# Optimization experiments

Measured on AMD Instinct MI355X. Metric: run time of the kernel, lower is better.

Reference implementation:

```python
import jax, jax.numpy as jnp
import numpy as np

TAU = 2.0   # LIF membrane time constant
VTH = 1.0   # spike threshold
EPS = 1e-5
T = 2       # spiking timesteps
H = 8       # attention heads
L = 4       # transformer depth
SCALE = 0.125
GW = 0.8    # graph branch weight


def _spike(v):
    # heaviside forward, sigmoid surrogate backward (spikingjelly-style)
    sg = jax.nn.sigmoid(4.0 * (v - VTH))
    return sg + jax.lax.stop_gradient((v >= VTH).astype(v.dtype) - sg)


def lif(x):
    # multi-step LIF over leading time axis, hard reset, detach_reset=True
    def step(v, xt):
        v = v + (xt - v) / TAU
        s = _spike(v)
        v = v * (1.0 - jax.lax.stop_gradient(s))
        return v, s
    _, s = jax.lax.scan(step, jnp.zeros_like(x[0]), x)
    return s


def bn(x, g, b):
    # batch-norm (training stats) over all dims but the channel dim
    ax = tuple(range(x.ndim - 1))
    m = x.mean(ax, keepdims=True)
    v = x.var(ax, keepdims=True)
    return (x - m) * jax.lax.rsqrt(v + EPS) * g + b


def ln(x, g, b):
    m = x.mean(-1, keepdims=True)
    v = x.var(-1, keepdims=True)
    return (x - m) * jax.lax.rsqrt(v + EPS) * g + b


def gcn_agg(x, row, col, n):
    # symmetric-normalized sparse aggregation: out[col] += x[row] / sqrt(d[row]d[col])
    deg = jax.ops.segment_sum(jnp.ones_like(col, dtype=x.dtype), col, num_segments=n)
    dinv = jnp.where(deg > 0, jax.lax.rsqrt(deg), 0.0)
    val = dinv[col] * dinv[row]
    return jax.ops.segment_sum(val[:, None] * x[row], col, num_segments=n)


def _forward(fl, edge_index):
    (x, fc0_w, fc0_b, ln_g, ln_b, wq, wk, wv, wo,
     bnq_g, bnq_b, bnk_g, bnk_b, bnv_g, bnv_b, bno_g, bno_b,
     w1, bn1_g, bn1_b, w2, bn2_g, bn2_b, head_w, head_b,
     gfc_w, gfc_b, gbn0_g, gbn0_b, gconv_w, gconv_b, gbn_g, gbn_b,
     fc_w, fc_b) = fl
    N = x.shape[0]
    row, col = edge_index[0], edge_index[1]
    # ---- spiking transformer branch: x -> [T,N,D] ----
    h = jnp.broadcast_to(x, (T,) + x.shape) @ fc0_w + fc0_b
    h = jax.nn.relu(ln(h, ln_g, ln_b))
    D = h.shape[-1]
    for l in range(L):
        s = lif(h)
        q = lif(bn(s @ wq[l], bnq_g[l], bnq_b[l])).reshape(T, N, H, D // H)
        k = lif(bn(s @ wk[l], bnk_g[l], bnk_b[l])).reshape(T, N, H, D // H)
        v = lif(bn(s @ wv[l], bnv_g[l], bnv_b[l])).reshape(T, N, H, D // H)
        # linear (token-sum) spiking self-attention: kv = K^T V per head/timestep
        kv = jnp.einsum('tnhd,tnhe->thde', k, v)
        o = (jnp.einsum('tnhd,thde->tnhe', q, kv) * SCALE).reshape(T, N, D)
        o = bn(lif(o) @ wo[l], bno_g[l], bno_b[l])
        h = h + o
        m = bn(lif(h) @ w1[l], bn1_g[l], bn1_b[l])
        m = bn(lif(m) @ w2[l], bn2_g[l], bn2_b[l])
        h = h + m
    x1 = (lif(h) @ head_w + head_b).mean(0)   # [N, C], mean over T (TET=False)
    # ---- sparse GNN diffusion branch ----
    g0 = jax.nn.relu(bn(x @ gfc_w + gfc_b, gbn0_g, gbn0_b))
    g = g0
    for i in range(2):
        g = gcn_agg(g, row, col, N) @ gconv_w[i] + gconv_b[i]
        g = jax.nn.relu(bn(g, gbn_g[i], gbn_b[i]))
        g = g + g0  # residual to first layer
    out = GW * g + (1.0 - GW) * x1
    return out @ fc_w + fc_b


def setup_inputs() -> dict:
    key = jax.random.key(0)
    ks = iter(jax.random.split(key, 64))
    N, F, D, C = 16384, 512, 512, 40
    DH = 2 * D
    r = lambda *s: jax.random.normal(next(ks), s, dtype=jnp.float32)
    inp = {
        'x': r(N, F),
        'fc0_w': r(F, D) * 0.02, 'fc0_b': jnp.zeros((D,), jnp.float32),
        'ln_g': jnp.ones((D,), jnp.float32), 'ln_b': jnp.zeros((D,), jnp.float32),
        'wq': r(L, D, D) * 0.02, 'wk': r(L, D, D) * 0.02,
        'wv': r(L, D, D) * 0.02, 'wo': r(L, D, D) * 0.02,
        'bnq_g': 1.0 + 0.1 * r(L, D), 'bnq_b': 0.02 * r(L, D),
        'bnk_g': 1.0 + 0.1 * r(L, D), 'bnk_b': 0.02 * r(L, D),
        'bnv_g': 1.0 + 0.1 * r(L, D), 'bnv_b': 0.02 * r(L, D),
        'bno_g': 1.0 + 0.1 * r(L, D), 'bno_b': 0.02 * r(L, D),
        'w1': r(L, D, DH) * 0.02, 'bn1_g': 1.0 + 0.1 * r(L, DH), 'bn1_b': 0.02 * r(L, DH),
        'w2': r(L, DH, D) * 0.02, 'bn2_g': 1.0 + 0.1 * r(L, D), 'bn2_b': 0.02 * r(L, D),
        'head_w': r(D, C) * 0.02, 'head_b': jnp.zeros((C,), jnp.float32),
        'gfc_w': r(F, C) * 0.02, 'gfc_b': jnp.zeros((C,), jnp.float32),
        'gbn0_g': jnp.ones((C,), jnp.float32), 'gbn0_b': jnp.zeros((C,), jnp.float32),
        'gconv_w': r(2, C, C) * 0.1, 'gconv_b': jnp.zeros((2, C), jnp.float32),
        'gbn_g': 1.0 + 0.1 * r(2, C), 'gbn_b': 0.02 * r(2, C),
        'fc_w': r(C, C) * 0.1, 'fc_b': jnp.zeros((C,), jnp.float32),
        'edge_index': jax.random.randint(next(ks), (2, 262144), 0, N, dtype=jnp.int32),
    }
    return inp


def reference(x, fc0_w, fc0_b, ln_g, ln_b, wq, wk, wv, wo, bnq_g, bnq_b, bnk_g, bnk_b, bnv_g, bnv_b, bno_g, bno_b, w1, bn1_g, bn1_b, w2, bn2_g, bn2_b, head_w, head_b, gfc_w, gfc_b, gbn0_g, gbn0_b, gconv_w, gconv_b, gbn_g, gbn_b, fc_w, fc_b, edge_index):
    fl = (x, fc0_w, fc0_b, ln_g, ln_b, wq, wk, wv, wo, bnq_g, bnq_b, bnk_g, bnk_b, bnv_g, bnv_b, bno_g, bno_b, w1, bn1_g, bn1_b, w2, bn2_g, bn2_b, head_w, head_b, gfc_w, gfc_b, gbn0_g, gbn0_b, gconv_w, gconv_b, gbn_g, gbn_b, fc_w, fc_b)
    return _forward(fl, edge_index)
```

## Files before the change

### kernel.cpp

```cpp
#include <hip/hip_runtime.h>
#include <cstddef>
#include <cstdint>

constexpr int N_NODES = 16384;
constexpr int D_MODEL = 512;
constexpr int C_OUT   = 40;
constexpr int CW      = 256;
constexpr int ND      = N_NODES * D_MODEL;
constexpr int M2      = 2 * N_NODES;

typedef int i32x4 __attribute__((ext_vector_type(4)));

#define S0 0.001953125
#define S1 1.52587890625e-05
#define S2 1.1920928955078125e-07
#define S3 9.31322574615478515625e-10
#define S4 7.2759576141834259033203125e-12

#define WD_Q 0
#define WD_K 1310720
#define WD_V 2621440
#define WD_O 3932160
#define WD_1 5242880
#define WD_2 7864320
#define WD_TOTAL 10485760

__global__ __launch_bounds__(256)
void w_digits_layer(const float* __restrict__ wq, const float* __restrict__ wk,
                    const float* __restrict__ wv, const float* __restrict__ wo,
                    const float* __restrict__ w1, const float* __restrict__ w2,
                    uint8_t* __restrict__ Wd) {
    int idx = blockIdx.x * 256 + threadIdx.x;
    const float* W;
    uint8_t* outb;
    int N, rem;
    if (idx < 65536) {
        int mm = idx >> 14;
        rem = idx & 16383;
        const float* ptrs[4] = {wq, wk, wv, wo};
        W = ptrs[mm]; outb = Wd + (size_t)mm * 1310720; N = 512;
    } else if (idx < 98304) {
        rem = idx - 65536; W = w1; outb = Wd + WD_1; N = 1024;
    } else {
        rem = idx - 98304; W = w2; outb = Wd + WD_2; N = 512;
    }
    int kg = rem / N, n = rem - kg * N;
    const float* Wp = W + (size_t)kg * 16 * N + n;
    uint8_t* out = outb + (size_t)(kg * N + n) * 80;
    const double scl[5] = {512.0, 65536.0, 8388608.0, 1073741824.0, 137438953472.0};
    const double inv[5] = {S0, S1, S2, S3, S4};
    union { uint8_t b[5][16]; i32x4 v[5]; } db;
#pragma unroll
    for (int kk = 0; kk < 16; ++kk) {
        double r = (double)Wp[(size_t)kk * N];
#pragma unroll
        for (int j = 0; j < 5; ++j) {
            int d = (int)rint(r * scl[j]);
            d = d > 127 ? 127 : (d < -127 ? -127 : d);
            r -= (double)d * inv[j];
            db.b[j][kk] = (uint8_t)(int8_t)d;
        }
    }
#pragma unroll
    for (int j = 0; j < 5; ++j)
        *reinterpret_cast<i32x4*>(out + j * 16) = db.v[j];
}

__global__ __launch_bounds__(256)
void gemm_i8_bits(const uint64_t* __restrict__ bits, int kWords,
                  const uint8_t* __restrict__ Wd, int Nmat, int colOff,
                  double* __restrict__ C, int ldc, int K,
                  double* __restrict__ sum, double* __restrict__ sumsq) {
    __shared__ __attribute__((aligned(16))) uint8_t Bs[20480];
    const int lane = threadIdx.x & 63;
    const int wv   = threadIdx.x >> 6;
    const int m    = lane & 15;
    const int q    = lane >> 4;
    const int rowT = blockIdx.y * 128 + wv * 32;
    const int colB = blockIdx.x * 64;

    i32x4 acc[2][4][5];
#pragma unroll
    for (int rt = 0; rt < 2; ++rt)
#pragma unroll
        for (int t = 0; t < 4; ++t)
#pragma unroll
            for (int j = 0; j < 5; ++j) acc[rt][t][j] = (i32x4){0, 0, 0, 0};

    const uint64_t* brow0 = bits + (size_t)(rowT + m) * kWords;
    const uint64_t* brow1 = brow0 + (size_t)16 * kWords;
    const size_t cb = (size_t)(colOff + colB);

    for (int kb = 0; kb < K; kb += 64) {
        i32x4 tmp[5];
        const size_t kt0 = (size_t)(kb >> 4);
#pragma unroll
        for (int c5 = 0; c5 < 5; ++c5) {
            int c  = threadIdx.x + c5 * 256;
            int kt = c / 320;
            int of = c - kt * 320;
            tmp[c5] = *reinterpret_cast<const i32x4*>(
                Wd + ((kt0 + (size_t)kt) * Nmat + cb) * 80 + (size_t)of * 16);
        }
        uint64_t wb0 = brow0[kb >> 6];
        uint64_t wb1 = brow1[kb >> 6];
        uint32_t hw0 = (uint32_t)(wb0 >> (q * 16)) & 0xFFFFu;
        uint32_t hw1 = (uint32_t)(wb1 >> (q * 16)) & 0xFFFFu;
        i32x4 af0, af1;
#pragma unroll
        for (int i = 0; i < 4; ++i) {
            af0[i] = (int)((((hw0 >> (4 * i)) & 0xFu) * 0x00204081u) & 0x01010101u);
            af1[i] = (int)((((hw1 >> (4 * i)) & 0xFu) * 0x00204081u) & 0x01010101u);
        }
        __syncthreads();
#pragma unroll
        for (int c5 = 0; c5 < 5; ++c5) {
            int c  = threadIdx.x + c5 * 256;
            int kt = c / 320;
            int of = c - kt * 320;
            *reinterpret_cast<i32x4*>(Bs + kt * 5120 + of * 16) = tmp[c5];
        }
        __syncthreads();
#pragma unroll
        for (int t = 0; t < 4; ++t) {
            const uint8_t* bt = Bs + q * 5120 + (t * 16 + m) * 80;
            i32x4 bf[5];
#pragma unroll
            for (int j = 0; j < 5; ++j)
                bf[j] = *reinterpret_cast<const i32x4*>(bt + j * 16);
#pragma unroll
            for (int j = 0; j < 5; ++j) {
                acc[0][t][j] = __builtin_amdgcn_mfma_i32_16x16x64_i8(af0, bf[j], acc[0][t][j], 0, 0, 0);
                acc[1][t][j] = __builtin_amdgcn_mfma_i32_16x16x64_i8(af1, bf[j], acc[1][t][j], 0, 0, 0);
            }
        }
    }

    double sarr[4], qarr[4];
#pragma unroll
    for (int t = 0; t < 4; ++t) { sarr[t] = 0.0; qarr[t] = 0.0; }
#pragma unroll
    for (int rt = 0; rt < 2; ++rt) {
        const int orow = rowT + rt * 16 + q * 4;
#pragma unroll
        for (int t = 0; t < 4; ++t) {
            double* Cc = C + (size_t)orow * ldc + colB + t * 16 + m;
#pragma unroll
            for (int i = 0; i < 4; ++i) {
                double p = (double)acc[rt][t][0][i] * S0 + (double)acc[rt][t][1][i] * S1
                         + (double)acc[rt][t][2][i] * S2 + (double)acc[rt][t][3][i] * S3
                         + (double)acc[rt][t][4][i] * S4;
                Cc[(size_t)i * ldc] = p;
                sarr[t] += p; qarr[t] += p * p;
            }
        }
    }
    __shared__ double ls[4][64], lq[4][64];
#pragma unroll
    for (int t = 0; t < 4; ++t) {
        double s = sarr[t], qq = qarr[t];
        s  += __shfl_xor(s, 16);  s  += __shfl_xor(s, 32);
        qq += __shfl_xor(qq, 16); qq += __shfl_xor(qq, 32);
        if (lane < 16) { ls[wv][t * 16 + lane] = s; lq[wv][t * 16 + lane] = qq; }
    }
    __syncthreads();
    if (threadIdx.x < 64) {
        int t = threadIdx.x;
        double s  = ls[0][t] + ls[1][t] + ls[2][t] + ls[3][t];
        double qq = lq[0][t] + lq[1][t] + lq[2][t] + lq[3][t];
        atomicAdd(&sum[colB + t], s);
        atomicAdd(&sumsq[colB + t], qq);
    }
}

__global__ __launch_bounds__(256)
void head_gather(const uint64_t* __restrict__ bits, const float* __restrict__ W,
                 const float* __restrict__ bias, float* __restrict__ Y) {
    const int lane = threadIdx.x & 63;
    const int wid  = threadIdx.x >> 6;
    const int r = blockIdx.x * 4 + wid;
    if (lane >= C_OUT) return;
    double acc = (double)bias[lane];
    const uint64_t* bw = bits + (size_t)r * 8;
    for (int j = 0; j < 8; ++j) {
        uint64_t w = bw[j];
        const float* Wk = W + (size_t)j * 64 * C_OUT + lane;
        while (w) {
            int k = __builtin_ctzll(w);
            w &= w - 1;
            acc += (double)Wk[(size_t)k * C_OUT];
        }
    }
    Y[(size_t)r * C_OUT + lane] = (float)acc;
}

__global__ __launch_bounds__(256)
void gemm_f32d(const float* __restrict__ A, int lda,
               const float* __restrict__ B, int ldb,
               const float* __restrict__ bias,
               double* __restrict__ C, int ldc, int M, int Nc, int K) {
    __shared__ double As[16][64];
    __shared__ double Bs[16][64];
    const int tid = threadIdx.x;
    const int tx  = tid & 15, ty = tid >> 4;
    const int row0 = blockIdx.y * 64 + ty * 4;
    const int col0 = blockIdx.x * 64 + tx * 4;
    const int ar = tid >> 2, ak = (tid & 3) * 4;
    const int bk = tid >> 4, bn = (tid & 15) * 4;
    const int gm = blockIdx.y * 64 + ar;
    double acc[4][4];
#pragma unroll
    for (int i = 0; i < 4; i++)
#pragma unroll
        for (int j = 0; j < 4; j++) acc[i][j] = 0.0;
    for (int k0 = 0; k0 < K; k0 += 16) {
#pragma unroll
        for (int j = 0; j < 4; j++)
            As[ak + j][ar] = (gm < M) ? (double)A[(size_t)gm * lda + k0 + ak + j] : 0.0;
#pragma unroll
        for (int j = 0; j < 4; j++) {
            int gn = blockIdx.x * 64 + bn + j;
            Bs[bk][bn + j] = (gn < Nc) ? (double)B[(size_t)(k0 + bk) * ldb + gn] : 0.0;
        }
        __syncthreads();
#pragma unroll
        for (int kk = 0; kk < 16; kk++) {
            double a4[4], b4[4];
#pragma unroll
            for (int i = 0; i < 4; i++) a4[i] = As[kk][ty * 4 + i];
#pragma unroll
            for (int j = 0; j < 4; j++) b4[j] = Bs[kk][tx * 4 + j];
#pragma unroll
            for (int i = 0; i < 4; i++)
#pragma unroll
                for (int j = 0; j < 4; j++) acc[i][j] = fma(a4[i], b4[j], acc[i][j]);
        }
        __syncthreads();
    }
#pragma unroll
    for (int i = 0; i < 4; i++) {
        int r = row0 + i;
        if (r >= M) continue;
#pragma unroll
        for (int j = 0; j < 4; j++) {
            int c = col0 + j;
            if (c < Nc) {
                double v = acc[i][j];
                if (bias) v += (double)bias[c];
                C[(size_t)r * ldc + c] = v;
            }
        }
    }
}

__global__ __launch_bounds__(256)
void gemm_f32(const float* __restrict__ A, int lda,
              const float* __restrict__ B, int ldb,
              const float* __restrict__ bias,
              float* __restrict__ C, int ldc, int M, int Nc, int K) {
    __shared__ float As[16][64];
    __shared__ float Bs[16][64];
    const int tid = threadIdx.x;
    const int tx  = tid & 15, ty = tid >> 4;
    const int row0 = blockIdx.y * 64 + ty * 4;
    const int col0 = blockIdx.x * 64 + tx * 4;
    const int ar = tid >> 2, ak = (tid & 3) * 4;
    const int bk = tid >> 4, bn = (tid & 15) * 4;
    const int gm = blockIdx.y * 64 + ar;
    double acc[4][4];
#pragma unroll
    for (int i = 0; i < 4; i++)
#pragma unroll
        for (int j = 0; j < 4; j++) acc[i][j] = 0.0;
    for (int k0 = 0; k0 < K; k0 += 16) {
#pragma unroll
        for (int j = 0; j < 4; j++) {
            int kk = k0 + ak + j;
            As[ak + j][ar] = (gm < M && kk < K) ? A[(size_t)gm * lda + kk] : 0.f;
        }
#pragma unroll
        for (int j = 0; j < 4; j++) {
            int gn = blockIdx.x * 64 + bn + j;
            int kk = k0 + bk;
            Bs[bk][bn + j] = (gn < Nc && kk < K) ? B[(size_t)kk * ldb + gn] : 0.f;
        }
        __syncthreads();
#pragma unroll
        for (int kk = 0; kk < 16; kk++) {
            float a4[4], b4[4];
#pragma unroll
            for (int i = 0; i < 4; i++) a4[i] = As[kk][ty * 4 + i];
#pragma unroll
            for (int j = 0; j < 4; j++) b4[j] = Bs[kk][tx * 4 + j];
#pragma unroll
            for (int i = 0; i < 4; i++)
#pragma unroll
                for (int j = 0; j < 4; j++) acc[i][j] = fma((double)a4[i], (double)b4[j], acc[i][j]);
        }
        __syncthreads();
    }
#pragma unroll
    for (int i = 0; i < 4; i++) {
        int r = row0 + i;
        if (r >= M) continue;
#pragma unroll
        for (int j = 0; j < 4; j++) {
            int c = col0 + j;
            if (c < Nc) {
                double v = acc[i][j];
                if (bias) v += (double)bias[c];
                C[(size_t)r * ldc + c] = (float)v;
            }
        }
    }
}

__global__ __launch_bounds__(256)
void col_stats_f(const float* __restrict__ X, int M, int Ch, int rowsPerBlock,
                 double* __restrict__ sum, double* __restrict__ sumsq) {
    const int cl = threadIdx.x & 63;
    const int c  = blockIdx.x * 64 + cl;
    const int rg = threadIdx.x >> 6;
    const int r0 = blockIdx.y * rowsPerBlock;
    const int r1 = min(r0 + rowsPerBlock, M);
    double s = 0.0, q = 0.0;
    if (c < Ch) {
        for (int r = r0 + rg; r < r1; r += 4) {
            double v = (double)X[(size_t)r * Ch + c];
            s += v; q += v * v;
        }
    }
    __shared__ double ls[4][64], lq[4][64];
    ls[rg][cl] = s; lq[rg][cl] = q;
    __syncthreads();
    if (rg == 0 && c < Ch) {
        s = ls[0][cl] + ls[1][cl] + ls[2][cl] + ls[3][cl];
        q = lq[0][cl] + lq[1][cl] + lq[2][cl] + lq[3][cl];
        atomicAdd(&sum[c], s);
        atomicAdd(&sumsq[c], q);
    }
}

__device__ __forceinline__ void lif2(double x0, double x1, bool& s0, bool& s1) {
    double v = x0 * 0.5;
    s0 = (v >= 1.0);
    v = s0 ? 0.0 : v;
    v = v + (x1 - v) * 0.5;
    s1 = (v >= 1.0);
}

__device__ __forceinline__ void bn_params(const double* sum, const double* sumsq,
                                          const float* g, const float* b, double invM,
                                          int c, double& sc, double& sh) {
    double m   = sum[c] * invM;
    double var = sumsq[c] * invM - m * m;
    sc = (double)g[c] / sqrt(var + 1e-5);
    sh = (double)b[c] - m * sc;
}

__global__ __launch_bounds__(256)
void lif_bits_f(const float* __restrict__ O, uint64_t* __restrict__ S) {
    int i = blockIdx.x * 256 + threadIdx.x;
    bool s0, s1;
    lif2((double)O[i], (double)O[(size_t)i + ND], s0, s1);
    uint64_t b0 = __ballot(s0), b1 = __ballot(s1);
    if ((threadIdx.x & 63) == 0) {
        int widx = i >> 6;
        S[widx] = b0;
        S[widx + N_NODES * 8] = b1;
    }
}

__global__ __launch_bounds__(256)
void bn_lif_bits2(const double* __restrict__ X,
                  const double* __restrict__ sum, const double* __restrict__ sumsq,
                  const float* __restrict__ g, const float* __restrict__ b, double invM,
                  uint64_t* __restrict__ S, int osWords, int chOffWords) {
    int i = blockIdx.x * 256 + threadIdx.x;
    int n = i >> 8, c = i & 255;
    double sc, sh;
    bn_params(sum, sumsq, g, b, invM, c, sc, sh);
    bool s0, s1;
    lif2((double)X[i] * sc + sh, (double)X[(size_t)i + (size_t)N_NODES * 256] * sc + sh, s0, s1);
    uint64_t b0 = __ballot(s0), b1 = __ballot(s1);
    if ((threadIdx.x & 63) == 0) {
        int widx = n * osWords + chOffWords + (c >> 6);
        S[widx] = b0;
        S[widx + N_NODES * osWords] = b1;
    }
}

__global__ __launch_bounds__(256)
void bn_add_lif2(const double* __restrict__ X,
                 const double* __restrict__ sum, const double* __restrict__ sumsq,
                 const float* __restrict__ g, const float* __restrict__ b, double invM,
                 double* __restrict__ H, int chOff, uint64_t* __restrict__ S) {
    int i = blockIdx.x * 256 + threadIdx.x;
    int n = i >> 8, c = i & 255;
    double sc, sh;
    bn_params(sum, sumsq, g, b, invM, c, sc, sh);
    size_t hi = (size_t)n * 512 + chOff + c;
    double h0 = H[hi] + ((double)X[i] * sc + sh);
    double h1 = H[hi + ND] + ((double)X[(size_t)i + (size_t)N_NODES * 256] * sc + sh);
    H[hi] = h0;
    H[hi + ND] = h1;
    bool s0, s1;
    lif2(h0, h1, s0, s1);
    uint64_t b0 = __ballot(s0), b1 = __ballot(s1);
    if ((threadIdx.x & 63) == 0) {
        int widx = n * 8 + (chOff >> 6) + (c >> 6);
        S[widx] = b0;
        S[widx + N_NODES * 8] = b1;
    }
}

__global__ __launch_bounds__(256)
void ln_relu_lif(const double* __restrict__ X, const float* __restrict__ g,
                 const float* __restrict__ b, double* __restrict__ H,
                 uint64_t* __restrict__ S) {
    int n = blockIdx.x;
    const double* x = X + (size_t)n * 512;
    int c0 = threadIdx.x, c1 = threadIdx.x + 256;
    double v0 = x[c0], v1 = x[c1];
    __shared__ double ls[256], lq[256];
    ls[threadIdx.x] = v0 + v1;
    lq[threadIdx.x] = v0 * v0 + v1 * v1;
    __syncthreads();
    for (int off = 128; off > 0; off >>= 1) {
        if (threadIdx.x < off) {
            ls[threadIdx.x] += ls[threadIdx.x + off];
            lq[threadIdx.x] += lq[threadIdx.x + off];
        }
        __syncthreads();
    }
    double m    = ls[0] * (1.0 / 512);
    double var  = lq[0] * (1.0 / 512) - m * m;
    double rstd = 1.0 / sqrt(var + 1e-5);
    double o0 = (v0 - m) * rstd * (double)g[c0] + (double)b[c0];
    double o1 = (v1 - m) * rstd * (double)g[c1] + (double)b[c1];
    o0 = o0 > 0.0 ? o0 : 0.0;
    o1 = o1 > 0.0 ? o1 : 0.0;
    double* h0 = H + (size_t)n * 512;
    h0[c0] = o0; h0[c1] = o1;
    h0[ND + c0] = o0; h0[ND + c1] = o1;
    bool a0, a1, d0, d1;
    lif2(o0, o0, a0, a1);
    lif2(o1, o1, d0, d1);
    uint64_t ba0 = __ballot(a0), ba1 = __ballot(a1);
    uint64_t bd0 = __ballot(d0), bd1 = __ballot(d1);
    if ((threadIdx.x & 63) == 0) {
        int w = threadIdx.x >> 6;
        S[n * 8 + w] = ba0;
        S[n * 8 + w + N_NODES * 8] = ba1;
        S[n * 8 + 4 + w] = bd0;
        S[n * 8 + 4 + w + N_NODES * 8] = bd1;
    }
}

__global__ __launch_bounds__(256)
void kv_bits(const uint64_t* __restrict__ Kb, const uint64_t* __restrict__ Vb,
             float* __restrict__ KV, int nPerBlock) {
    const int th = blockIdx.x;
    const int t = th >> 3, h = th & 7;
    const int nbase = blockIdx.y * nPerBlock;
    const int e = threadIdx.x & 63, dg = threadIdx.x >> 6;
    float acc[16];
#pragma unroll
    for (int i = 0; i < 16; i++) acc[i] = 0.f;
    __shared__ float ks[8][64], vs[8][64];
    const size_t wbase = (size_t)t * N_NODES * 8 + h;
    for (int n0 = 0; n0 < nPerBlock; n0 += 8) {
        for (int idx = threadIdx.x; idx < 8 * 128; idx += 256) {
            int r = idx >> 7, c = idx & 127;
            size_t wi = wbase + (size_t)(nbase + n0 + r) * 8;
            if (c < 64) ks[r][c] = (float)((Kb[wi] >> c) & 1ull);
            else        vs[r][c - 64] = (float)((Vb[wi] >> (c - 64)) & 1ull);
        }
        __syncthreads();
#pragma unroll
        for (int r = 0; r < 8; ++r) {
            float ve = vs[r][e];
#pragma unroll
            for (int i = 0; i < 16; ++i) acc[i] += ks[r][dg * 16 + i] * ve;
        }
        __syncthreads();
    }
    float* kvp = KV + (size_t)th * 4096;
    for (int i = 0; i < 16; ++i)
        atomicAdd(&kvp[(dg * 16 + i) * 64 + e], acc[i]);
}

__global__ __launch_bounds__(256)
void o_bits(const uint64_t* __restrict__ Qb, const float* __restrict__ KV,
            float* __restrict__ O) {
    const int th = blockIdx.y;
    const int t = th >> 3, h = th & 7;
    const int nb = blockIdx.x;
    __shared__ float kvs[64][64];
    __shared__ float qs[64][65];
    const float* kvp = KV + (size_t)th * 4096;
    for (int idx = threadIdx.x; idx < 4096; idx += 256)
        kvs[idx >> 6][idx & 63] = kvp[idx];
    const size_t wbase = ((size_t)t * N_NODES + (size_t)nb * 64) * 8 + h;
    for (int idx = threadIdx.x; idx < 4096; idx += 256) {
        int r = idx >> 6, c = idx & 63;
        qs[r][c] = (float)((Qb[wbase + (size_t)r * 8] >> c) & 1ull);
    }
    __syncthreads();
    const int e = threadIdx.x & 63, rg = threadIdx.x >> 6;
    float acc[16];
#pragma unroll
    for (int i = 0; i < 16; i++) acc[i] = 0.f;
    for (int d = 0; d < 64; ++d) {
        float kv = kvs[d][e];
#pragma unroll
        for (int i = 0; i < 16; ++i) acc[i] += qs[rg * 16 + i][d] * kv;
    }
    const size_t obase = ((size_t)t * N_NODES + (size_t)nb * 64) * 512 + (size_t)h * 64;
    for (int i = 0; i < 16; ++i)
        O[obase + (size_t)(rg * 16 + i) * 512 + e] = acc[i] * 0.125f;
}

__global__ __launch_bounds__(256)
void deg_kernel(const int* __restrict__ col, float* __restrict__ deg, int E) {
    int e = blockIdx.x * 256 + threadIdx.x;
    if (e < E) atomicAdd(&deg[col[e]], 1.0f);
}

__global__ __launch_bounds__(256)
void dinv_kernel(float* __restrict__ deg, int n) {
    int i = blockIdx.x * 256 + threadIdx.x;
    if (i < n) {
        double d = (double)deg[i];
        deg[i] = d > 0.0 ? (float)(1.0 / sqrt(d)) : 0.f;
    }
}

__global__ __launch_bounds__(256)
void agg_kernel(const float* __restrict__ G, const int* __restrict__ row,
                const int* __restrict__ col, const float* __restrict__ dinv,
                float* __restrict__ out, int E) {
    int idx = blockIdx.x * 256 + threadIdx.x;
    int e = idx >> 6, c = idx & 63;
    if (e >= E || c >= C_OUT) return;
    int r = row[e], cl = col[e];
    float val = dinv[cl] * dinv[r];
    atomicAdd(&out[(size_t)cl * C_OUT + c], val * G[(size_t)r * C_OUT + c]);
}

__global__ __launch_bounds__(256)
void bn_relu_add_f2(const float* __restrict__ X,
                    const double* __restrict__ sum, const double* __restrict__ sumsq,
                    const float* __restrict__ g, const float* __restrict__ b, double invM,
                    const float* __restrict__ add, float* __restrict__ out, int NC, int Ch) {
    int i = blockIdx.x * 256 + threadIdx.x;
    if (i >= NC) return;
    int c = i % Ch;
    double sc, sh;
    bn_params(sum, sumsq, g, b, invM, c, sc, sh);
    double v = (double)X[i] * sc + sh;
    v = v > 0.0 ? v : 0.0;
    if (add) v += (double)add[i];
    out[i] = (float)v;
}

__global__ __launch_bounds__(256)
void mix_kernel(const float* __restrict__ G, const float* __restrict__ Y,
                float* __restrict__ P, int NC) {
    int i = blockIdx.x * 256 + threadIdx.x;
    if (i >= NC) return;
    double y = 0.5 * ((double)Y[i] + (double)Y[(size_t)i + NC]);
    P[i] = (float)(0.8 * (double)G[i] + 0.2 * y);
}

__global__ __launch_bounds__(256)
void final_fc_kernel(const float* __restrict__ A, const float* __restrict__ W,
                     const float* __restrict__ bias, float* __restrict__ out) {
    __shared__ float Ws[40][40];
    for (int idx = threadIdx.x; idx < 1600; idx += 256)
        Ws[idx / 40][idx % 40] = W[idx];
    __syncthreads();
    int i = blockIdx.x * 256 + threadIdx.x;
    if (i >= N_NODES * C_OUT) return;
    int n = i / 40, c = i - n * 40;
    const float* a = A + (size_t)n * 40;
    double acc = (double)bias[c];
#pragma unroll 8
    for (int k = 0; k < 40; ++k) acc += (double)a[k] * (double)Ws[k][c];
    out[i] = (float)acc;
}

static inline dim3 grid1(long n) { return dim3((unsigned)((n + 255) / 256)); }

extern "C" void kernel_launch(void* const* d_in, const int* in_sizes, int n_in,
                              void* d_out, int out_size, void* d_ws, size_t ws_size,
                              hipStream_t stream) {
    const float* x      = (const float*)d_in[0];
    const float* fc0_w  = (const float*)d_in[1];
    const float* fc0_b  = (const float*)d_in[2];
    const float* ln_g   = (const float*)d_in[3];
    const float* ln_b   = (const float*)d_in[4];
    const float* wq     = (const float*)d_in[5];
    const float* wk     = (const float*)d_in[6];
    const float* wv     = (const float*)d_in[7];
    const float* wo     = (const float*)d_in[8];
    const float* bnq_g  = (const float*)d_in[9];
    const float* bnq_b  = (const float*)d_in[10];
    const float* bnk_g  = (const float*)d_in[11];
    const float* bnk_b  = (const float*)d_in[12];
    const float* bnv_g  = (const float*)d_in[13];
    const float* bnv_b  = (const float*)d_in[14];
    const float* bno_g  = (const float*)d_in[15];
    const float* bno_b  = (const float*)d_in[16];
    const float* w1     = (const float*)d_in[17];
    const float* bn1_g  = (const float*)d_in[18];
    const float* bn1_b  = (const float*)d_in[19];
    const float* w2     = (const float*)d_in[20];
    const float* bn2_g  = (const float*)d_in[21];
    const float* bn2_b  = (const float*)d_in[22];
    const float* head_w = (const float*)d_in[23];
    const float* head_b = (const float*)d_in[24];
    const float* gfc_w  = (const float*)d_in[25];
    const float* gfc_b  = (const float*)d_in[26];
    const float* gbn0_g = (const float*)d_in[27];
    const float* gbn0_b = (const float*)d_in[28];
    const float* gconv_w= (const float*)d_in[29];
    const float* gconv_b= (const float*)d_in[30];
    const float* gbn_g  = (const float*)d_in[31];
    const float* gbn_b  = (const float*)d_in[32];
    const float* fc_w   = (const float*)d_in[33];
    const float* fc_b   = (const float*)d_in[34];
    const int*   edge   = (const int*)d_in[35];

    const int E = in_sizes[35] / 2;
    const int* erow = edge;
    const int* ecol = edge + E;
    const int NC = N_NODES * C_OUT;

    uint8_t* wsbase = (uint8_t*)d_ws;
    size_t off = 0;
    auto alloc = [&](size_t bytes, size_t align) -> void* {
        off = (off + align - 1) & ~(align - 1);
        void* p = wsbase + off;
        off += bytes;
        return p;
    };
    double*   statBuf = (double*)alloc((size_t)64 * 512 * sizeof(double), 256);
    double*   h_buf  = (double*)alloc((size_t)2 * ND * sizeof(double), 256);
    double*   Pd     = (double*)alloc((size_t)M2 * CW * sizeof(double), 256);
    float*    O32    = (float*)Pd;
    uint8_t*  Wdig   = (uint8_t*)alloc((size_t)WD_TOTAL, 256);
    uint64_t* s_bits = (uint64_t*)alloc((size_t)2 * N_NODES * 8 * 8, 256);
    uint64_t* q_bits = (uint64_t*)alloc((size_t)2 * N_NODES * 8 * 8, 256);
    uint64_t* k_bits = (uint64_t*)alloc((size_t)2 * N_NODES * 8 * 8, 256);
    uint64_t* v_bits = (uint64_t*)alloc((size_t)2 * N_NODES * 8 * 8, 256);
    uint64_t* m_bits = (uint64_t*)alloc((size_t)2 * N_NODES * 16 * 8, 256);
    float*    ybuf   = (float*)m_bits;
    (void)alloc((size_t)2 * NC * sizeof(float) > (size_t)2 * N_NODES * 16 * 8
                ? (size_t)2 * NC * sizeof(float) - (size_t)2 * N_NODES * 16 * 8 : 0, 256);
    float*    g0     = (float*)alloc((size_t)NC * sizeof(float), 256);
    float*    gg     = (float*)alloc((size_t)NC * sizeof(float), 256);
    float*    ag     = (float*)alloc((size_t)NC * sizeof(float), 256);
    float*    kvb    = (float*)alloc((size_t)65536 * sizeof(float), 256);
    float*    deg    = (float*)alloc((size_t)N_NODES * sizeof(float), 256);
    if (off > ws_size) return;

    const dim3 blk(256);
    const dim3 gLIF((unsigned)(ND / 256));
    const dim3 gCHK((unsigned)(N_NODES));
    const dim3 gGEMM(CW / 64, M2 / 128);
    const double invM2 = 1.0 / (double)M2;
    const double invMN = 1.0 / (double)N_NODES;

    hipMemsetAsync(statBuf, 0, (size_t)64 * 512 * sizeof(double), stream);

    int gate = 0;
    auto nextStat = [&]() { return statBuf + (size_t)(gate++) * 512; };

    hipLaunchKernelGGL(gemm_f32d, dim3(8, N_NODES / 64), blk, 0, stream,
                       x, 512, fc0_w, 512, fc0_b, Pd, 512, N_NODES, 512, 512);
    hipLaunchKernelGGL(ln_relu_lif, dim3(N_NODES), blk, 0, stream, Pd, ln_g, ln_b, h_buf, s_bits);

    for (int l = 0; l < 4; ++l) {
        hipLaunchKernelGGL(w_digits_layer, dim3(512), blk, 0, stream,
                           wq + (size_t)l * 262144, wk + (size_t)l * 262144,
                           wv + (size_t)l * 262144, wo + (size_t)l * 262144,
                           w1 + (size_t)l * 524288, w2 + (size_t)l * 524288, Wdig);

        uint64_t* qkvb[3] = {q_bits, k_bits, v_bits};
        const size_t wdoff[3] = {WD_Q, WD_K, WD_V};
        const float* gmat[3] = {bnq_g + l * 512, bnk_g + l * 512, bnv_g + l * 512};
        const float* bmat[3] = {bnq_b + l * 512, bnk_b + l * 512, bnv_b + l * 512};
        for (int j = 0; j < 3; ++j) {
            for (int c0 = 0; c0 < 512; c0 += CW) {
                double* st = nextStat();
                hipLaunchKernelGGL(gemm_i8_bits, gGEMM, blk, 0, stream,
                                   s_bits, 8, Wdig + wdoff[j], 512, c0, Pd, CW, 512, st, st + 256);
                hipLaunchKernelGGL(bn_lif_bits2, gCHK, blk, 0, stream,
                                   Pd, st, st + 256, gmat[j] + c0, bmat[j] + c0, invM2,
                                   qkvb[j], 8, c0 / 64);
            }
        }

        hipMemsetAsync(kvb, 0, 65536 * sizeof(float), stream);
        hipLaunchKernelGGL(kv_bits, dim3(16, 16), blk, 0, stream, k_bits, v_bits, kvb, 1024);
        hipLaunchKernelGGL(o_bits, dim3(N_NODES / 64, 16), blk, 0, stream, q_bits, kvb, O32);
        hipLaunchKernelGGL(lif_bits_f, gLIF, blk, 0, stream, O32, q_bits);

        for (int c0 = 0; c0 < 512; c0 += CW) {
            double* st = nextStat();
            hipLaunchKernelGGL(gemm_i8_bits, gGEMM, blk, 0, stream,
                               q_bits, 8, Wdig + WD_O, 512, c0, Pd, CW, 512, st, st + 256);
            hipLaunchKernelGGL(bn_add_lif2, gCHK, blk, 0, stream,
                               Pd, st, st + 256, bno_g + l * 512 + c0, bno_b + l * 512 + c0,
                               invM2, h_buf, c0, s_bits);
        }

        for (int c0 = 0; c0 < 1024; c0 += CW) {
            double* st = nextStat();
            hipLaunchKernelGGL(gemm_i8_bits, gGEMM, blk, 0, stream,
                               s_bits, 8, Wdig + WD_1, 1024, c0, Pd, CW, 512, st, st + 256);
            hipLaunchKernelGGL(bn_lif_bits2, gCHK, blk, 0, stream,
                               Pd, st, st + 256, bn1_g + l * 1024 + c0, bn1_b + l * 1024 + c0,
                               invM2, m_bits, 16, c0 / 64);
        }
        for (int c0 = 0; c0 < 512; c0 += CW) {
            double* st = nextStat();
            hipLaunchKernelGGL(gemm_i8_bits, gGEMM, blk, 0, stream,
                               m_bits, 16, Wdig + WD_2, 512, c0, Pd, CW, 1024, st, st + 256);
            hipLaunchKernelGGL(bn_add_lif2, gCHK, blk, 0, stream,
                               Pd, st, st + 256, bn2_g + l * 512 + c0, bn2_b + l * 512 + c0,
                               invM2, h_buf, c0, s_bits);
        }
    }

    hipLaunchKernelGGL(head_gather, dim3(M2 / 4), blk, 0, stream, s_bits, head_w, head_b, ybuf);

    hipLaunchKernelGGL(gemm_f32, dim3(1, N_NODES / 64), blk, 0, stream,
                       x, 512, gfc_w, 40, gfc_b, ag, 40, N_NODES, 40, 512);
    {
        double* st = nextStat();
        dim3 gs(1, (N_NODES + 511) / 512);
        hipLaunchKernelGGL(col_stats_f, gs, blk, 0, stream, ag, N_NODES, 40, 512, st, st + 256);
        hipLaunchKernelGGL(bn_relu_add_f2, grid1(NC), blk, 0, stream,
                           ag, st, st + 256, gbn0_g, gbn0_b, invMN,
                           (const float*)nullptr, g0, NC, 40);
    }

    hipMemsetAsync(deg, 0, N_NODES * sizeof(float), stream);
    hipLaunchKernelGGL(deg_kernel, grid1(E), blk, 0, stream, ecol, deg, E);
    hipLaunchKernelGGL(dinv_kernel, grid1(N_NODES), blk, 0, stream, deg, N_NODES);

    const float* gsrc = g0;
    for (int i = 0; i < 2; ++i) {
        hipMemsetAsync(ag, 0, (size_t)NC * sizeof(float), stream);
        hipLaunchKernelGGL(agg_kernel, grid1((long)E * 64), blk, 0, stream,
                           gsrc, erow, ecol, deg, ag, E);
        hipLaunchKernelGGL(gemm_f32, dim3(1, N_NODES / 64), blk, 0, stream,
                           ag, 40, gconv_w + (size_t)i * 40 * 40, 40, gconv_b + i * 40,
                           gg, 40, N_NODES, 40, 40);
        double* st = nextStat();
        dim3 gs(1, (N_NODES + 511) / 512);
        hipLaunchKernelGGL(col_stats_f, gs, blk, 0, stream, gg, N_NODES, 40, 512, st, st + 256);
        hipLaunchKernelGGL(bn_relu_add_f2, grid1(NC), blk, 0, stream,
                           gg, st, st + 256, gbn_g + i * 40, gbn_b + i * 40, invMN, g0, gg, NC, 40);
        gsrc = gg;
    }

    hipLaunchKernelGGL(mix_kernel, grid1(NC), blk, 0, stream, gg, ybuf, ag, NC);
    hipLaunchKernelGGL(final_fc_kernel, grid1((long)N_NODES * C_OUT), blk, 0, stream,
                       ag, fc_w, fc_b, (float*)d_out);
}
```

Measured before the change: 6.726 ms.

## Fuse attention output with LIF spiking and use float shared tiles in fp32 GEMM

The attention output kernel now handles both timesteps for a head in one block. It applies the LIF spike directly and writes spike bits in place, so the separate float output buffer and the LIF pass over it are no longer needed. The input GEMM now stages tiles in float shared memory with vectorized loads and XOR swizzling, while still accumulating in double. Its bounds checks are dropped, which relies on the dimensions dividing evenly. The kv accumulation tile also grows from 8 to 16 rows per step.

```diff
diff --git a/kernel.cpp b/kernel.cpp
--- a/kernel.cpp
+++ b/kernel.cpp
@@ -199,8 +199,8 @@
                const float* __restrict__ B, int ldb,
                const float* __restrict__ bias,
                double* __restrict__ C, int ldc, int M, int Nc, int K) {
-    __shared__ double As[16][64];
-    __shared__ double Bs[16][64];
+    __shared__ float As[16][64];
+    __shared__ float Bs[16][64];
     const int tid = threadIdx.x;
     const int tx  = tid & 15, ty = tid >> 4;
     const int row0 = blockIdx.y * 64 + ty * 4;
@@ -214,26 +214,26 @@
 #pragma unroll
         for (int j = 0; j < 4; j++) acc[i][j] = 0.0;
     for (int k0 = 0; k0 < K; k0 += 16) {
+        float4 av = *reinterpret_cast<const float4*>(&A[(size_t)gm * lda + k0 + ak]);
+        const float* avp = reinterpret_cast<const float*>(&av);
 #pragma unroll
         for (int j = 0; j < 4; j++)
-            As[ak + j][ar] = (gm < M) ? (double)A[(size_t)gm * lda + k0 + ak + j] : 0.0;
-#pragma unroll
-        for (int j = 0; j < 4; j++) {
-            int gn = blockIdx.x * 64 + bn + j;
-            Bs[bk][bn + j] = (gn < Nc) ? (double)B[(size_t)(k0 + bk) * ldb + gn] : 0.0;
-        }
+            As[ak + j][ar ^ ((ak + j) & 12)] = avp[j];
+        float4 bv = *reinterpret_cast<const float4*>(
+            &B[(size_t)(k0 + bk) * ldb + blockIdx.x * 64 + bn]);
+        *reinterpret_cast<float4*>(&Bs[bk][bn ^ ((bk & 3) << 2)]) = bv;
         __syncthreads();
 #pragma unroll
         for (int kk = 0; kk < 16; kk++) {
-            double a4[4], b4[4];
-#pragma unroll
-            for (int i = 0; i < 4; i++) a4[i] = As[kk][ty * 4 + i];
-#pragma unroll
-            for (int j = 0; j < 4; j++) b4[j] = Bs[kk][tx * 4 + j];
+            float4 a4 = *reinterpret_cast<const float4*>(&As[kk][(ty * 4) ^ (kk & 12)]);
+            float4 b4 = *reinterpret_cast<const float4*>(&Bs[kk][(tx * 4) ^ ((kk & 3) << 2)]);
+            const float* ap = reinterpret_cast<const float*>(&a4);
+            const float* bp = reinterpret_cast<const float*>(&b4);
 #pragma unroll
             for (int i = 0; i < 4; i++)
 #pragma unroll
-                for (int j = 0; j < 4; j++) acc[i][j] = fma(a4[i], b4[j], acc[i][j]);
+                for (int j = 0; j < 4; j++)
+                    acc[i][j] = fma((double)ap[i], (double)bp[j], acc[i][j]);
         }
         __syncthreads();
     }
@@ -356,19 +356,6 @@
     double var = sumsq[c] * invM - m * m;
     sc = (double)g[c] / sqrt(var + 1e-5);
     sh = (double)b[c] - m * sc;
-}
-
-__global__ __launch_bounds__(256)
-void lif_bits_f(const float* __restrict__ O, uint64_t* __restrict__ S) {
-    int i = blockIdx.x * 256 + threadIdx.x;
-    bool s0, s1;
-    lif2((double)O[i], (double)O[(size_t)i + ND], s0, s1);
-    uint64_t b0 = __ballot(s0), b1 = __ballot(s1);
-    if ((threadIdx.x & 63) == 0) {
-        int widx = i >> 6;
-        S[widx] = b0;
-        S[widx + N_NODES * 8] = b1;
-    }
 }
 
 __global__ __launch_bounds__(256)
@@ -467,10 +454,10 @@
     float acc[16];
 #pragma unroll
     for (int i = 0; i < 16; i++) acc[i] = 0.f;
-    __shared__ float ks[8][64], vs[8][64];
+    __shared__ float ks[16][64], vs[16][64];
     const size_t wbase = (size_t)t * N_NODES * 8 + h;
-    for (int n0 = 0; n0 < nPerBlock; n0 += 8) {
-        for (int idx = threadIdx.x; idx < 8 * 128; idx += 256) {
+    for (int n0 = 0; n0 < nPerBlock; n0 += 16) {
+        for (int idx = threadIdx.x; idx < 16 * 128; idx += 256) {
             int r = idx >> 7, c = idx & 127;
             size_t wi = wbase + (size_t)(nbase + n0 + r) * 8;
             if (c < 64) ks[r][c] = (float)((Kb[wi] >> c) & 1ull);
@@ -478,7 +465,7 @@
         }
         __syncthreads();
 #pragma unroll
-        for (int r = 0; r < 8; ++r) {
+        for (int r = 0; r < 16; ++r) {
             float ve = vs[r][e];
 #pragma unroll
             for (int i = 0; i < 16; ++i) acc[i] += ks[r][dg * 16 + i] * ve;
@@ -491,34 +478,48 @@
 }
 
 __global__ __launch_bounds__(256)
-void o_bits(const uint64_t* __restrict__ Qb, const float* __restrict__ KV,
-            float* __restrict__ O) {
-    const int th = blockIdx.y;
-    const int t = th >> 3, h = th & 7;
+void o_lif_bits(const uint64_t* __restrict__ Qb, const float* __restrict__ KV,
+                uint64_t* __restrict__ S) {
+    const int h  = blockIdx.y;
     const int nb = blockIdx.x;
     __shared__ float kvs[64][64];
     __shared__ float qs[64][65];
-    const float* kvp = KV + (size_t)th * 4096;
-    for (int idx = threadIdx.x; idx < 4096; idx += 256)
-        kvs[idx >> 6][idx & 63] = kvp[idx];
-    const size_t wbase = ((size_t)t * N_NODES + (size_t)nb * 64) * 8 + h;
-    for (int idx = threadIdx.x; idx < 4096; idx += 256) {
-        int r = idx >> 6, c = idx & 63;
-        qs[r][c] = (float)((Qb[wbase + (size_t)r * 8] >> c) & 1ull);
-    }
-    __syncthreads();
     const int e = threadIdx.x & 63, rg = threadIdx.x >> 6;
-    float acc[16];
-#pragma unroll
-    for (int i = 0; i < 16; i++) acc[i] = 0.f;
-    for (int d = 0; d < 64; ++d) {
-        float kv = kvs[d][e];
-#pragma unroll
-        for (int i = 0; i < 16; ++i) acc[i] += qs[rg * 16 + i][d] * kv;
-    }
-    const size_t obase = ((size_t)t * N_NODES + (size_t)nb * 64) * 512 + (size_t)h * 64;
-    for (int i = 0; i < 16; ++i)
-        O[obase + (size_t)(rg * 16 + i) * 512 + e] = acc[i] * 0.125f;
+    float acc0[16], acc1[16];
+#pragma unroll
+    for (int i = 0; i < 16; ++i) { acc0[i] = 0.f; acc1[i] = 0.f; }
+#pragma unroll
+    for (int t = 0; t < 2; ++t) {
+        const float* kvp = KV + (size_t)(t * 8 + h) * 4096;
+        for (int idx = threadIdx.x; idx < 4096; idx += 256)
+            kvs[idx >> 6][idx & 63] = kvp[idx];
+        const size_t wbase = ((size_t)t * N_NODES + (size_t)nb * 64) * 8 + h;
+        for (int idx = threadIdx.x; idx < 4096; idx += 256) {
+            int r = idx >> 6, c = idx & 63;
+            qs[r][c] = (float)((Qb[wbase + (size_t)r * 8] >> c) & 1ull);
+        }
+        __syncthreads();
+        float* acc = t == 0 ? acc0 : acc1;
+        for (int d = 0; d < 64; ++d) {
+            float kv = kvs[d][e];
+#pragma unroll
+            for (int i = 0; i < 16; ++i) acc[i] += qs[rg * 16 + i][d] * kv;
+        }
+        __syncthreads();
+    }
+#pragma unroll
+    for (int i = 0; i < 16; ++i) {
+        float o0 = acc0[i] * 0.125f;
+        float o1 = acc1[i] * 0.125f;
+        bool s0, s1;
+        lif2((double)o0, (double)o1, s0, s1);
+        uint64_t b0 = __ballot(s0), b1 = __ballot(s1);
+        if (e == 0) {
+            size_t row = (size_t)nb * 64 + rg * 16 + i;
+            S[row * 8 + h] = b0;
+            S[row * 8 + h + (size_t)N_NODES * 8] = b1;
+        }
+    }
 }
 
 __global__ __launch_bounds__(256)
@@ -648,7 +649,6 @@
     double*   statBuf = (double*)alloc((size_t)64 * 512 * sizeof(double), 256);
     double*   h_buf  = (double*)alloc((size_t)2 * ND * sizeof(double), 256);
     double*   Pd     = (double*)alloc((size_t)M2 * CW * sizeof(double), 256);
-    float*    O32    = (float*)Pd;
     uint8_t*  Wdig   = (uint8_t*)alloc((size_t)WD_TOTAL, 256);
     uint64_t* s_bits = (uint64_t*)alloc((size_t)2 * N_NODES * 8 * 8, 256);
     uint64_t* q_bits = (uint64_t*)alloc((size_t)2 * N_NODES * 8 * 8, 256);
@@ -666,7 +666,6 @@
     if (off > ws_size) return;
 
     const dim3 blk(256);
-    const dim3 gLIF((unsigned)(ND / 256));
     const dim3 gCHK((unsigned)(N_NODES));
     const dim3 gGEMM(CW / 64, M2 / 128);
     const double invM2 = 1.0 / (double)M2;
@@ -704,8 +703,7 @@
 
         hipMemsetAsync(kvb, 0, 65536 * sizeof(float), stream);
         hipLaunchKernelGGL(kv_bits, dim3(16, 16), blk, 0, stream, k_bits, v_bits, kvb, 1024);
-        hipLaunchKernelGGL(o_bits, dim3(N_NODES / 64, 16), blk, 0, stream, q_bits, kvb, O32);
-        hipLaunchKernelGGL(lif_bits_f, gLIF, blk, 0, stream, O32, q_bits);
+        hipLaunchKernelGGL(o_lif_bits, dim3(N_NODES / 64, 8), blk, 0, stream, q_bits, kvb, q_bits);
 
         for (int c0 = 0; c0 < 512; c0 += CW) {
             double* st = nextStat();
```

Measured after the change: 6.605 ms. About the same (-1.8%).
